# Kernel optimization log

Measured on AMD Instinct MI355X. Metric: run time of the kernel, lower is better.

## Reference

```python
import jax, jax.numpy as jnp
import numpy as np

# Baked genome DAG structure (static per-instance in the original module)
N_IN = 256
LAYER_SIZES = [256, 256, 256, 256, 64]  # 4 hidden layers + output layer
N_OUT = LAYER_SIZES[-1]
N_EVAL = sum(LAYER_SIZES)  # 1088 eval nodes (node_evals)
DEG = 32                   # incoming links per eval node
BATCH = 8192


def setup_inputs() -> dict:
    key = jax.random.key(0)
    kx, kw, kb, kr = jax.random.split(key, 4)
    x = jax.random.normal(kx, (BATCH, N_IN), dtype=jnp.float32)
    # connection weights, node bias, node response (learned genome params)
    w = jax.random.normal(kw, (N_EVAL, DEG), dtype=jnp.float32) * 0.5
    bias = jax.random.normal(kb, (N_EVAL,), dtype=jnp.float32) * 0.1
    response = 1.0 + jax.random.normal(kr, (N_EVAL,), dtype=jnp.float32) * 0.1
    # per-layer source indices: each eval node connects to DEG earlier nodes
    src_rows = []
    offset = N_IN  # number of nodes topologically before current layer
    for li, sz in enumerate(LAYER_SIZES):
        ks = jax.random.fold_in(key, 100 + li)
        src_rows.append(jax.random.randint(ks, (sz, DEG), 0, offset, dtype=jnp.int32))
        offset += sz
    src_idx = jnp.concatenate(src_rows, axis=0)  # [N_EVAL, DEG]
    return {"x": x, "w": w, "bias": bias, "response": response, "src_idx": src_idx}


def reference(x, w, bias, response, src_idx):
    # values: [B, n_nodes_so_far]; starts as the input node values
    values = x
    row = 0
    for sz in LAYER_SIZES:  # small fixed structural loop (topological layers)
        s = src_idx[row:row + sz]                       # [sz, DEG]
        gathered = values[:, s]                         # [B, sz, DEG]
        agg = jnp.einsum('bsd,sd->bs', gathered, w[row:row + sz])  # sum aggregation
        out = jax.nn.relu(bias[row:row + sz] + response[row:row + sz] * agg)
        values = jnp.concatenate([values, out], axis=1)
        row += sz
    return values[:, -N_OUT:]  # [B, N_OUT]
```

## Files before the change

kernel.cpp:

```cpp
#include <hip/hip_runtime.h>

#define N_IN   256
#define N_EVAL 1088
#define TOTALW 1344
#define DEG    32

typedef __attribute__((ext_vector_type(8))) short short8;
typedef __attribute__((ext_vector_type(4))) float f32x4;
typedef unsigned short u16;
typedef unsigned int   u32;

__device__ __forceinline__ u32 pk2(float lo, float hi) {
    u32 ul = __float_as_uint(lo);
    u32 uh = __float_as_uint(hi);
    ul = (ul + 0x7fffu + ((ul >> 16) & 1u)) >> 16;
    uh = (uh + 0x7fffu + ((uh >> 16) & 1u)) & 0xffff0000u;
    return ul | uh;
}
__device__ __forceinline__ u16 bf1(float v) {
    u32 u = __float_as_uint(v);
    return (u16)((u + 0x7fffu + ((u >> 16) & 1u)) >> 16);
}

__global__ __launch_bounds__(256) void build_dense4(
    const int* __restrict__ src, const float* __restrict__ w,
    u16* __restrict__ B)
{
    int t = blockIdx.x * 256 + threadIdx.x;
    int g  = t / 23040;
    int tt = t - g * 23040;
    int li, nloc, kt, base, NT;
    if      (tt < 2048)  { li = 0; int r = tt;         nloc = r >> 3; kt = r & 7;  base = 0;      NT = 16; }
    else if (tt < 6144)  { li = 1; int r = tt - 2048;  nloc = r >> 4; kt = r & 15; base = 65536;  NT = 16; }
    else if (tt < 12288) { li = 2; int r = tt - 6144;  nloc = r / 24; kt = r % 24; base = 196608; NT = 16; }
    else if (tt < 20480) { li = 3; int r = tt - 12288; nloc = r >> 5; kt = r & 31; base = 393216; NT = 16; }
    else                 { li = 4; int r = tt - 20480; nloc = r / 40; kt = r % 40; base = 655360; NT = 4;  }
    const int gn = li * 256 + nloc;

    int c[DEG]; float ow[DEG];
    const int4*   s4 = (const int4*)(src + (size_t)gn * DEG);
    const float4* w4 = (const float4*)(w   + (size_t)gn * DEG);
    #pragma unroll
    for (int k = 0; k < 8; ++k) {
        int4 ci = s4[k]; float4 wf = w4[k];
        c[4*k+0]=ci.x; c[4*k+1]=ci.y; c[4*k+2]=ci.z; c[4*k+3]=ci.w;
        ow[4*k+0]=wf.x; ow[4*k+1]=wf.y; ow[4*k+2]=wf.z; ow[4*k+3]=wf.w;
    }
    const int k0 = kt * 32 + g * 8;
    float v[8];
    #pragma unroll
    for (int kk = 0; kk < 8; ++kk) {
        float s = 0.f;
        #pragma unroll
        for (int d = 0; d < DEG; ++d)
            s += (c[d] == k0 + kk) ? ow[d] : 0.f;
        v[kk] = s;
    }
    const int nt = nloc >> 4, ln = nloc & 15;
    const int lane = (g << 4) | ln;
    const int idx  = base + ((kt * NT + nt) * 64 + lane) * 8;
    uint4 pk = make_uint4(pk2(v[0], v[1]), pk2(v[2], v[3]),
                          pk2(v[4], v[5]), pk2(v[6], v[7]));
    *(uint4*)(B + idx) = pk;
}

#define TILE_B 32
#define LDSCOLS 1280
#define RSTRIDE (LDSCOLS * 2)

#define MFMA(a, b, c) __builtin_amdgcn_mfma_f32_16x16x32_bf16(a, b, c, 0, 0, 0)

__global__ __launch_bounds__(512) void neat_mfma(
    const float* __restrict__ x, const u16* __restrict__ Bbuf,
    const float* __restrict__ bias, const float* __restrict__ resp,
    float* __restrict__ out)
{
    __shared__ uint4 ldsq[(TILE_B * RSTRIDE) / 16];
    __shared__ f32x4 pbuf[4 * 64 * 2];
    char* lds = (char*)ldsq;
    const int tid  = threadIdx.x;
    const int b0   = blockIdx.x * TILE_B;
    const int lane = tid & 63;
    const int wvid = tid >> 6;

    const short8* Bf = (const short8*)Bbuf;
    const short8* pre0 = Bf + wvid * 64 + lane;
    const short8* pre1 = Bf + (wvid + 8) * 64 + lane;
    short8 L00 = pre0[0], L01 = pre0[1024], L02 = pre0[2048], L03 = pre0[3072];
    short8 L10 = pre1[0], L11 = pre1[1024], L12 = pre1[2048], L13 = pre1[3072];

    #pragma unroll
    for (int i = 0; i < 4; ++i) {
        int f4 = tid + i * 512;
        int row = f4 >> 6;
        int c4  = f4 & 63;
        float4 xv = ((const float4*)(x + (size_t)(b0 + row) * N_IN))[c4];
        u32 p0 = pk2(xv.x, xv.y), p1 = pk2(xv.z, xv.w);
        int byte = row * RSTRIDE + ((c4 * 8) ^ ((row & 7) << 4));
        *(u32*)(lds + byte)     = p0;
        *(u32*)(lds + byte + 4) = p1;
    }
    __syncthreads();

    const int r0  = lane & 15;
    const int g16 = (lane >> 4) << 4;
    const int sw  = (r0 & 7) << 4;
    const int ab0 = r0 * RSTRIDE;
    const int ab1 = (r0 + 16) * RSTRIDE;

    int cbase = N_IN;
    #pragma unroll
    for (int li = 0; li < 5; ++li) {
        const int ktn = (N_IN + li * 256) >> 5;
        const int loff8[5] = {0, 8192, 24576, 49152, 81920};
        const int lo8 = loff8[li];
        const int nbase = cbase - N_IN;

        if (li < 4) {
            const int STEP = 16 * 64;
            const int nt0 = wvid, nt1 = wvid + 8;
            f32x4 acc00 = {0,0,0,0}, acc01 = {0,0,0,0};
            f32x4 acc10 = {0,0,0,0}, acc11 = {0,0,0,0};
            const short8* bp0 = Bf + lo8 + nt0 * 64 + lane;
            const short8* bp1 = Bf + lo8 + nt1 * 64 + lane;
            short8 p00, p01, p02, p03, p10, p11, p12, p13;
            if (li == 0) {
                p00 = L00; p01 = L01; p02 = L02; p03 = L03;
                p10 = L10; p11 = L11; p12 = L12; p13 = L13;
            } else {
                p00 = bp0[0]; p01 = bp0[STEP]; p02 = bp0[2*STEP]; p03 = bp0[3*STEP];
                p10 = bp1[0]; p11 = bp1[STEP]; p12 = bp1[2*STEP]; p13 = bp1[3*STEP];
            }
            for (int kt4 = 0; kt4 < ktn; kt4 += 4) {
                #pragma unroll
                for (int j = 0; j < 4; ++j) {
                    int kt  = kt4 + j;
                    int ktp = kt + 4; if (ktp >= ktn) ktp = ktn - 1;
                    short8 f0 = bp0[ktp * STEP];
                    short8 f1 = bp1[ktp * STEP];
                    int inrow = (kt * 64 + g16) ^ sw;
                    short8 a0 = *(const short8*)(lds + ab0 + inrow);
                    short8 a1 = *(const short8*)(lds + ab1 + inrow);
                    short8 b0v = (j == 0) ? p00 : (j == 1) ? p01 : (j == 2) ? p02 : p03;
                    short8 b1v = (j == 0) ? p10 : (j == 1) ? p11 : (j == 2) ? p12 : p13;
                    acc00 = MFMA(a0, b0v, acc00);
                    acc01 = MFMA(a1, b0v, acc01);
                    acc10 = MFMA(a0, b1v, acc10);
                    acc11 = MFMA(a1, b1v, acc11);
                    if      (j == 0) { p00 = f0; p10 = f1; }
                    else if (j == 1) { p01 = f0; p11 = f1; }
                    else if (j == 2) { p02 = f0; p12 = f1; }
                    else             { p03 = f0; p13 = f1; }
                }
            }
            #pragma unroll
            for (int t = 0; t < 2; ++t) {
                int nt = t ? nt1 : nt0;
                f32x4 aA = t ? acc10 : acc00;
                f32x4 aB = t ? acc11 : acc01;
                int gr = nbase + nt * 16 + r0;
                float bb = bias[gr], rr = resp[gr];
                int colbyte = (cbase + nt * 16 + r0) * 2;
                #pragma unroll
                for (int r = 0; r < 4; ++r) {
                    int i0 = ((lane >> 4) << 2) + r;
                    float v0 = fmaxf(fmaf(rr, aA[r], bb), 0.f);
                    *(u16*)(lds + i0 * RSTRIDE + (colbyte ^ ((i0 & 7) << 4))) = bf1(v0);
                    int i1 = i0 + 16;
                    float v1 = fmaxf(fmaf(rr, aB[r], bb), 0.f);
                    *(u16*)(lds + i1 * RSTRIDE + (colbyte ^ ((i1 & 7) << 4))) = bf1(v1);
                }
            }
            __syncthreads();
        } else {
            const int STEP = 4 * 64;
            const int nt0   = wvid & 3;
            const int ktbeg = (wvid >> 2) * 20;
            const int ktend = ktbeg + 20;
            f32x4 acc0 = {0,0,0,0}, acc1 = {0,0,0,0};
            const short8* bp0 = Bf + lo8 + nt0 * 64 + lane;
            short8 p00 = bp0[(ktbeg + 0) * STEP];
            short8 p01 = bp0[(ktbeg + 1) * STEP];
            short8 p02 = bp0[(ktbeg + 2) * STEP];
            short8 p03 = bp0[(ktbeg + 3) * STEP];
            for (int kt4 = ktbeg; kt4 < ktend; kt4 += 4) {
                #pragma unroll
                for (int j = 0; j < 4; ++j) {
                    int kt  = kt4 + j;
                    int ktp = kt + 4; if (ktp >= ktend) ktp = ktend - 1;
                    short8 f0 = bp0[ktp * STEP];
                    int inrow = (kt * 64 + g16) ^ sw;
                    short8 a0 = *(const short8*)(lds + ab0 + inrow);
                    short8 a1 = *(const short8*)(lds + ab1 + inrow);
                    short8 b0v = (j == 0) ? p00 : (j == 1) ? p01 : (j == 2) ? p02 : p03;
                    acc0 = MFMA(a0, b0v, acc0);
                    acc1 = MFMA(a1, b0v, acc1);
                    if      (j == 0) p00 = f0;
                    else if (j == 1) p01 = f0;
                    else if (j == 2) p02 = f0;
                    else             p03 = f0;
                }
            }
            if (wvid >= 4) {
                pbuf[((wvid - 4) * 64 + lane) * 2 + 0] = acc0;
                pbuf[((wvid - 4) * 64 + lane) * 2 + 1] = acc1;
            }
            __syncthreads();
            if (wvid < 4) {
                f32x4 q0 = pbuf[(wvid * 64 + lane) * 2 + 0];
                f32x4 q1 = pbuf[(wvid * 64 + lane) * 2 + 1];
                acc0 += q0; acc1 += q1;
                int gr = nbase + nt0 * 16 + r0;
                float bb = bias[gr], rr = resp[gr];
                int col = nt0 * 16 + r0;
                #pragma unroll
                for (int r = 0; r < 4; ++r) {
                    int i0 = ((lane >> 4) << 2) + r;
                    out[(size_t)(b0 + i0) * 64 + col] = fmaxf(fmaf(rr, acc0[r], bb), 0.f);
                    int i1 = i0 + 16;
                    out[(size_t)(b0 + i1) * 64 + col] = fmaxf(fmaf(rr, acc1[r], bb), 0.f);
                }
            }
        }
        cbase += 256;
    }
}

#define FTILE_B 16
__device__ __forceinline__ int gbyte(int c, int h) {
    return ((c << 5) + (h << 4)) ^ (int)((((unsigned)c >> 2) & 7u) << 5);
}
__device__ __forceinline__ void fmadw(u32 d, float wv, float* acc) {
    acc[0] = fmaf(__uint_as_float(d << 16), wv, acc[0]);
    acc[1] = fmaf(__uint_as_float(d & 0xffff0000u), wv, acc[1]);
}
__device__ __forceinline__ void colacc16(const u32* vals, int c, float wv, float* acc) {
    const uint4* p = (const uint4*)((const char*)vals + gbyte(c, 0));
    uint4 a = p[0]; uint4 b = p[1];
    fmadw(a.x, wv, acc + 0);  fmadw(a.y, wv, acc + 2);
    fmadw(a.z, wv, acc + 4);  fmadw(a.w, wv, acc + 6);
    fmadw(b.x, wv, acc + 8);  fmadw(b.y, wv, acc + 10);
    fmadw(b.z, wv, acc + 12); fmadw(b.w, wv, acc + 14);
}
__global__ __launch_bounds__(256) void neat_eval_r4(
    const float* __restrict__ x, const float* __restrict__ w,
    const float* __restrict__ bias, const float* __restrict__ resp,
    const int* __restrict__ src, float* __restrict__ out)
{
    __shared__ u32 vals[TOTALW * 8];
    const int tid = threadIdx.x;
    const int b0  = blockIdx.x * FTILE_B;
    #pragma unroll
    for (int i = 0; i < 2; ++i) {
        int g = tid + i * 256;
        int c = g & 255, h = g >> 8;
        u32 pk[4];
        #pragma unroll
        for (int j = 0; j < 4; ++j) {
            float lo = x[(size_t)(b0 + h * 8 + 2 * j    ) * N_IN + c];
            float hi = x[(size_t)(b0 + h * 8 + 2 * j + 1) * N_IN + c];
            pk[j] = pk2(lo, hi);
        }
        *(uint4*)((char*)vals + gbyte(c, h)) = make_uint4(pk[0], pk[1], pk[2], pk[3]);
    }
    __syncthreads();
    int row = 0, outoff = N_IN;
    #pragma unroll
    for (int li = 0; li < 5; ++li) {
        const int sz = (li < 4) ? 256 : 64;
        for (int n = tid; n < sz; n += 256) {
            const int gr = row + n;
            const int4*   s4 = (const int4*)(src + (size_t)gr * DEG);
            const float4* w4 = (const float4*)(w   + (size_t)gr * DEG);
            float acc[16];
            #pragma unroll
            for (int i = 0; i < 16; ++i) acc[i] = 0.f;
            #pragma unroll
            for (int k = 0; k < DEG / 4; ++k) {
                int4 i4 = s4[k]; float4 wv = w4[k];
                colacc16(vals, i4.x, wv.x, acc);
                colacc16(vals, i4.y, wv.y, acc);
                colacc16(vals, i4.z, wv.z, acc);
                colacc16(vals, i4.w, wv.w, acc);
            }
            const float bb = bias[gr], rr = resp[gr];
            u32 pk[8];
            #pragma unroll
            for (int j = 0; j < 8; ++j) {
                float lo = fmaxf(fmaf(rr, acc[2 * j    ], bb), 0.f);
                float hi = fmaxf(fmaf(rr, acc[2 * j + 1], bb), 0.f);
                pk[j] = pk2(lo, hi);
            }
            int ob = gbyte(outoff + n, 0);
            *(uint4*)((char*)vals + ob)      = make_uint4(pk[0], pk[1], pk[2], pk[3]);
            *(uint4*)((char*)vals + ob + 16) = make_uint4(pk[4], pk[5], pk[6], pk[7]);
        }
        __syncthreads();
        row += sz; outoff += sz;
    }
    #pragma unroll
    for (int i = 0; i < 4; ++i) {
        int idx = tid + i * 256;
        int c = idx & 63, b = idx >> 6;
        int col = TOTALW - 64 + c;
        const u32* g = (const u32*)((const char*)vals + gbyte(col, b >> 3));
        u32 d = g[(b & 7) >> 1];
        float v = (b & 1) ? __uint_as_float(d & 0xffff0000u)
                          : __uint_as_float(d << 16);
        out[(size_t)(b0 + b) * 64 + c] = v;
    }
}

extern "C" void kernel_launch(void* const* d_in, const int* in_sizes, int n_in,
                              void* d_out, int out_size, void* d_ws, size_t ws_size,
                              hipStream_t stream) {
    const float* x    = (const float*)d_in[0];
    const float* w    = (const float*)d_in[1];
    const float* bias = (const float*)d_in[2];
    const float* resp = (const float*)d_in[3];
    const int*   src  = (const int*)d_in[4];
    float* out = (float*)d_out;

    const int batch = in_sizes[0] / N_IN;
    const size_t need = 737280ull * 2;

    if (ws_size >= need && (batch % TILE_B) == 0) {
        u16* Bbuf = (u16*)d_ws;
        build_dense4<<<360, 256, 0, stream>>>(src, w, Bbuf);
        neat_mfma<<<batch / TILE_B, 512, 0, stream>>>(x, Bbuf, bias, resp, out);
    } else {
        neat_eval_r4<<<batch / FTILE_B, 256, 0, stream>>>(x, w, bias, resp, src, out);
    }
}
```

Baseline: 30.09 us.

## Deepen weight prefetch to eight k-tiles and parallelize dense weight build

The dense bf16 weight build kernel now has each thread produce one packed pair instead of eight values, so it launches four times as many threads with shorter per-thread loops, which should cut the prep kernel's latency. In the MFMA kernel, the B-operand register prefetch ring for hidden layers grows from 4 to 8 k-tiles, using register arrays indexed by the unrolled loop. Bias and response loads are hoisted ahead of the k-loop so their latency overlaps the matrix work. The deeper prefetch raises VGPR pressure, which could lower occupancy or cause spills.

```diff
diff --git a/kernel.cpp b/kernel.cpp
--- a/kernel.cpp
+++ b/kernel.cpp
@@ -22,20 +22,28 @@
     return (u16)((u + 0x7fffu + ((u >> 16) & 1u)) >> 16);
 }
 
-__global__ __launch_bounds__(256) void build_dense4(
+__global__ __launch_bounds__(256) void build_dense32(
     const int* __restrict__ src, const float* __restrict__ w,
-    u16* __restrict__ B)
+    u32* __restrict__ B32)
 {
-    int t = blockIdx.x * 256 + threadIdx.x;
-    int g  = t / 23040;
-    int tt = t - g * 23040;
-    int li, nloc, kt, base, NT;
-    if      (tt < 2048)  { li = 0; int r = tt;         nloc = r >> 3; kt = r & 7;  base = 0;      NT = 16; }
-    else if (tt < 6144)  { li = 1; int r = tt - 2048;  nloc = r >> 4; kt = r & 15; base = 65536;  NT = 16; }
-    else if (tt < 12288) { li = 2; int r = tt - 6144;  nloc = r / 24; kt = r % 24; base = 196608; NT = 16; }
-    else if (tt < 20480) { li = 3; int r = tt - 12288; nloc = r >> 5; kt = r & 31; base = 393216; NT = 16; }
-    else                 { li = 4; int r = tt - 20480; nloc = r / 40; kt = r % 40; base = 655360; NT = 4;  }
-    const int gn = li * 256 + nloc;
+    const int t = blockIdx.x * 256 + threadIdx.x;
+    const int tile = t >> 8;
+    const int q    = t & 255;
+    const int lane = q >> 2;
+    const int e2   = q & 3;
+    int li, ts;
+    if      (tile < 128)  { li = 0; ts = 0;    }
+    else if (tile < 384)  { li = 1; ts = 128;  }
+    else if (tile < 768)  { li = 2; ts = 384;  }
+    else if (tile < 1280) { li = 3; ts = 768;  }
+    else                  { li = 4; ts = 1280; }
+    const int tloc = tile - ts;
+    int kt, nt;
+    if (li < 4) { kt = tloc >> 4; nt = tloc & 15; }
+    else        { kt = tloc >> 2; nt = tloc & 3;  }
+    const int ln = lane & 15, g = lane >> 4;
+    const int gn = li * 256 + nt * 16 + ln;
+    const int k0 = kt * 32 + g * 8 + e2 * 2;
 
     int c[DEG]; float ow[DEG];
     const int4*   s4 = (const int4*)(src + (size_t)gn * DEG);
@@ -46,22 +54,13 @@
         c[4*k+0]=ci.x; c[4*k+1]=ci.y; c[4*k+2]=ci.z; c[4*k+3]=ci.w;
         ow[4*k+0]=wf.x; ow[4*k+1]=wf.y; ow[4*k+2]=wf.z; ow[4*k+3]=wf.w;
     }
-    const int k0 = kt * 32 + g * 8;
-    float v[8];
-    #pragma unroll
-    for (int kk = 0; kk < 8; ++kk) {
-        float s = 0.f;
-        #pragma unroll
-        for (int d = 0; d < DEG; ++d)
-            s += (c[d] == k0 + kk) ? ow[d] : 0.f;
-        v[kk] = s;
-    }
-    const int nt = nloc >> 4, ln = nloc & 15;
-    const int lane = (g << 4) | ln;
-    const int idx  = base + ((kt * NT + nt) * 64 + lane) * 8;
-    uint4 pk = make_uint4(pk2(v[0], v[1]), pk2(v[2], v[3]),
-                          pk2(v[4], v[5]), pk2(v[6], v[7]));
-    *(uint4*)(B + idx) = pk;
+    float s0 = 0.f, s1 = 0.f;
+    #pragma unroll
+    for (int d = 0; d < DEG; ++d) {
+        s0 += (c[d] == k0    ) ? ow[d] : 0.f;
+        s1 += (c[d] == k0 + 1) ? ow[d] : 0.f;
+    }
+    B32[t] = pk2(s0, s1);
 }
 
 #define TILE_B 32
@@ -84,10 +83,16 @@
     const int wvid = tid >> 6;
 
     const short8* Bf = (const short8*)Bbuf;
-    const short8* pre0 = Bf + wvid * 64 + lane;
-    const short8* pre1 = Bf + (wvid + 8) * 64 + lane;
-    short8 L00 = pre0[0], L01 = pre0[1024], L02 = pre0[2048], L03 = pre0[3072];
-    short8 L10 = pre1[0], L11 = pre1[1024], L12 = pre1[2048], L13 = pre1[3072];
+    short8 rp0[8], rp1[8];
+    {
+        const short8* bp0 = Bf + wvid * 64 + lane;
+        const short8* bp1 = Bf + (wvid + 8) * 64 + lane;
+        #pragma unroll
+        for (int j = 0; j < 8; ++j) {
+            rp0[j] = bp0[j * 1024];
+            rp1[j] = bp1[j * 1024];
+        }
+    }
 
     #pragma unroll
     for (int i = 0; i < 4; ++i) {
@@ -119,38 +124,37 @@
         if (li < 4) {
             const int STEP = 16 * 64;
             const int nt0 = wvid, nt1 = wvid + 8;
+            const short8* bp0 = Bf + lo8 + nt0 * 64 + lane;
+            const short8* bp1 = Bf + lo8 + nt1 * 64 + lane;
+            if (li != 0) {
+                #pragma unroll
+                for (int j = 0; j < 8; ++j) {
+                    rp0[j] = bp0[j * STEP];
+                    rp1[j] = bp1[j * STEP];
+                }
+            }
+            const int gr0 = nbase + nt0 * 16 + r0;
+            const int gr1 = nbase + nt1 * 16 + r0;
+            const float bb0 = bias[gr0], rr0 = resp[gr0];
+            const float bb1 = bias[gr1], rr1 = resp[gr1];
+
             f32x4 acc00 = {0,0,0,0}, acc01 = {0,0,0,0};
             f32x4 acc10 = {0,0,0,0}, acc11 = {0,0,0,0};
-            const short8* bp0 = Bf + lo8 + nt0 * 64 + lane;
-            const short8* bp1 = Bf + lo8 + nt1 * 64 + lane;
-            short8 p00, p01, p02, p03, p10, p11, p12, p13;
-            if (li == 0) {
-                p00 = L00; p01 = L01; p02 = L02; p03 = L03;
-                p10 = L10; p11 = L11; p12 = L12; p13 = L13;
-            } else {
-                p00 = bp0[0]; p01 = bp0[STEP]; p02 = bp0[2*STEP]; p03 = bp0[3*STEP];
-                p10 = bp1[0]; p11 = bp1[STEP]; p12 = bp1[2*STEP]; p13 = bp1[3*STEP];
-            }
-            for (int kt4 = 0; kt4 < ktn; kt4 += 4) {
-                #pragma unroll
-                for (int j = 0; j < 4; ++j) {
-                    int kt  = kt4 + j;
-                    int ktp = kt + 4; if (ktp >= ktn) ktp = ktn - 1;
+            for (int kt8 = 0; kt8 < ktn; kt8 += 8) {
+                #pragma unroll
+                for (int j = 0; j < 8; ++j) {
+                    int kt  = kt8 + j;
+                    int ktp = kt + 8; if (ktp >= ktn) ktp = ktn - 1;
                     short8 f0 = bp0[ktp * STEP];
                     short8 f1 = bp1[ktp * STEP];
                     int inrow = (kt * 64 + g16) ^ sw;
                     short8 a0 = *(const short8*)(lds + ab0 + inrow);
                     short8 a1 = *(const short8*)(lds + ab1 + inrow);
-                    short8 b0v = (j == 0) ? p00 : (j == 1) ? p01 : (j == 2) ? p02 : p03;
-                    short8 b1v = (j == 0) ? p10 : (j == 1) ? p11 : (j == 2) ? p12 : p13;
-                    acc00 = MFMA(a0, b0v, acc00);
-                    acc01 = MFMA(a1, b0v, acc01);
-                    acc10 = MFMA(a0, b1v, acc10);
-                    acc11 = MFMA(a1, b1v, acc11);
-                    if      (j == 0) { p00 = f0; p10 = f1; }
-                    else if (j == 1) { p01 = f0; p11 = f1; }
-                    else if (j == 2) { p02 = f0; p12 = f1; }
-                    else             { p03 = f0; p13 = f1; }
+                    acc00 = MFMA(a0, rp0[j], acc00);
+                    acc01 = MFMA(a1, rp0[j], acc01);
+                    acc10 = MFMA(a0, rp1[j], acc10);
+                    acc11 = MFMA(a1, rp1[j], acc11);
+                    rp0[j] = f0; rp1[j] = f1;
                 }
             }
             #pragma unroll
@@ -158,8 +162,8 @@
                 int nt = t ? nt1 : nt0;
                 f32x4 aA = t ? acc10 : acc00;
                 f32x4 aB = t ? acc11 : acc01;
-                int gr = nbase + nt * 16 + r0;
-                float bb = bias[gr], rr = resp[gr];
+                float bb = t ? bb1 : bb0;
+                float rr = t ? rr1 : rr0;
                 int colbyte = (cbase + nt * 16 + r0) * 2;
                 #pragma unroll
                 for (int r = 0; r < 4; ++r) {
@@ -177,12 +181,13 @@
             const int nt0   = wvid & 3;
             const int ktbeg = (wvid >> 2) * 20;
             const int ktend = ktbeg + 20;
+            const short8* bp0 = Bf + lo8 + nt0 * 64 + lane;
+            #pragma unroll
+            for (int j = 0; j < 4; ++j) rp0[j] = bp0[(ktbeg + j) * STEP];
+            const int gr0 = nbase + nt0 * 16 + r0;
+            const float bb0 = bias[gr0], rr0 = resp[gr0];
+
             f32x4 acc0 = {0,0,0,0}, acc1 = {0,0,0,0};
-            const short8* bp0 = Bf + lo8 + nt0 * 64 + lane;
-            short8 p00 = bp0[(ktbeg + 0) * STEP];
-            short8 p01 = bp0[(ktbeg + 1) * STEP];
-            short8 p02 = bp0[(ktbeg + 2) * STEP];
-            short8 p03 = bp0[(ktbeg + 3) * STEP];
             for (int kt4 = ktbeg; kt4 < ktend; kt4 += 4) {
                 #pragma unroll
                 for (int j = 0; j < 4; ++j) {
@@ -192,13 +197,9 @@
                     int inrow = (kt * 64 + g16) ^ sw;
                     short8 a0 = *(const short8*)(lds + ab0 + inrow);
                     short8 a1 = *(const short8*)(lds + ab1 + inrow);
-                    short8 b0v = (j == 0) ? p00 : (j == 1) ? p01 : (j == 2) ? p02 : p03;
-                    acc0 = MFMA(a0, b0v, acc0);
-                    acc1 = MFMA(a1, b0v, acc1);
-                    if      (j == 0) p00 = f0;
-                    else if (j == 1) p01 = f0;
-                    else if (j == 2) p02 = f0;
-                    else             p03 = f0;
+                    acc0 = MFMA(a0, rp0[j], acc0);
+                    acc1 = MFMA(a1, rp0[j], acc1);
+                    rp0[j] = f0;
                 }
             }
             if (wvid >= 4) {
@@ -210,15 +211,13 @@
                 f32x4 q0 = pbuf[(wvid * 64 + lane) * 2 + 0];
                 f32x4 q1 = pbuf[(wvid * 64 + lane) * 2 + 1];
                 acc0 += q0; acc1 += q1;
-                int gr = nbase + nt0 * 16 + r0;
-                float bb = bias[gr], rr = resp[gr];
                 int col = nt0 * 16 + r0;
                 #pragma unroll
                 for (int r = 0; r < 4; ++r) {
                     int i0 = ((lane >> 4) << 2) + r;
-                    out[(size_t)(b0 + i0) * 64 + col] = fmaxf(fmaf(rr, acc0[r], bb), 0.f);
+                    out[(size_t)(b0 + i0) * 64 + col] = fmaxf(fmaf(rr0, acc0[r], bb0), 0.f);
                     int i1 = i0 + 16;
-                    out[(size_t)(b0 + i1) * 64 + col] = fmaxf(fmaf(rr, acc1[r], bb), 0.f);
+                    out[(size_t)(b0 + i1) * 64 + col] = fmaxf(fmaf(rr0, acc1[r], bb0), 0.f);
                 }
             }
         }
@@ -325,9 +324,9 @@
     const size_t need = 737280ull * 2;
 
     if (ws_size >= need && (batch % TILE_B) == 0) {
-        u16* Bbuf = (u16*)d_ws;
-        build_dense4<<<360, 256, 0, stream>>>(src, w, Bbuf);
-        neat_mfma<<<batch / TILE_B, 512, 0, stream>>>(x, Bbuf, bias, resp, out);
+        u32* Bbuf = (u32*)d_ws;
+        build_dense32<<<1440, 256, 0, stream>>>(src, w, Bbuf);
+        neat_mfma<<<batch / TILE_B, 512, 0, stream>>>(x, (const u16*)Bbuf, bias, resp, out);
     } else {
         neat_eval_r4<<<batch / FTILE_B, 256, 0, stream>>>(x, w, bias, resp, src, out);
     }
```

Measured after the change: 29.56 us. About the same (-1.8%).
